# Optimization experiments

Hardware: AMD Instinct MI355X
Metric: run time of the kernel (lower is better)

## Reference

```python
import jax, jax.numpy as jnp
import numpy as np

E = 2048            # total edges in the batch
L = 8               # num_features == max_walk_length
G = 128             # num_graphs in the batch
HID = 128
N_NODES = 4096


def setup_inputs() -> dict:
    key = jax.random.key(0)
    k0, k1, k2, k3 = jax.random.split(key, 4)
    edge_index = jax.random.randint(k0, (2, E), 0, N_NODES, dtype=jnp.int32)
    edge_graph = jnp.sort(jax.random.randint(k1, (E,), 0, G, dtype=jnp.int32))
    W1 = jax.random.normal(k2, (L, HID), dtype=jnp.float32) * (1.0 / np.sqrt(L))
    b1 = jnp.zeros((HID,), dtype=jnp.float32)
    W2 = jax.random.normal(k3, (HID, 1), dtype=jnp.float32) * (1.0 / np.sqrt(HID))
    b2 = jnp.zeros((1,), dtype=jnp.float32)
    return {"edge_index": edge_index, "edge_graph": edge_graph,
            "W1": W1, "b1": b1, "W2": W2, "b2": b2}


def reference(edge_index, edge_graph, W1, b1, W2, b2):
    src, dst = edge_index[0], edge_index[1]  # edge i = (src_i, dst_i)
    # Non-backtracking edge matrix: B[i, j] = 1 iff dst_j == src_i and src_j != dst_i
    # (matches the python condition `u != l and v == k` with edge_i=(k,l), edge_j=(u,v))
    B = ((dst[None, :] == src[:, None]) & (src[None, :] != dst[:, None])).astype(jnp.float32)
    e = B.shape[0]
    walk_len = W1.shape[0]

    # B^1 .. B^L via scan, collecting diagonals (non-backtracking closed-walk counts per edge)
    def step(P, _):
        P = P @ B
        return P, jnp.diagonal(P)

    _, diags = jax.lax.scan(step, jnp.eye(e, dtype=jnp.float32), None, length=walk_len)
    # diags: [L, E] -> per-graph signatures [G, L]
    sig = jax.ops.segment_sum(diags.T, edge_graph, num_segments=G)

    # MLP (eval mode: dropout is identity)
    h = jax.nn.relu(sig @ W1 + b1)
    return h @ W2 + b2
```

## Files before the change

### kernel.cpp

```cpp
#include <hip/hip_runtime.h>


constexpr int E_EDGES  = 2048;
constexpr int L_WALK   = 8;
constexpr int G_GRAPHS = 128;
constexpr int HID      = 128;
constexpr int N_NODES  = 4096;
constexpr int BLOCK    = 1024;
constexpr int CAP      = 2048;

typedef unsigned long long u64;

__launch_bounds__(BLOCK, 1)
__global__ void nbc_all(const int* __restrict__ edge_index,
                        const int* __restrict__ edge_graph,
                        const float* __restrict__ W1,
                        const float* __restrict__ b1,
                        const float* __restrict__ W2,
                        const float* __restrict__ b2,
                        float* __restrict__ out)
{
    __shared__ u64 s_bufA[CAP];
    __shared__ u64 s_bufB[CAP];
    __shared__ u64 s_node[E_EDGES];
    __shared__ int s_sig[G_GRAPHS * L_WALK];
    __shared__ int s_nn[L_WALK + 1];
    __shared__ float s_W1[L_WALK * HID];
    __shared__ float s_b1[HID];
    __shared__ float s_W2[HID];
    __shared__ float s_b2;

    int* s_head = (int*)s_bufA;

    const int t    = threadIdx.x;
    const int lane = t & 63;

    const int2 se2 = ((const int2*)edge_index)[t];
    const int2 de2 = ((const int2*)(edge_index + E_EDGES))[t];
    const int2 ge2 = ((const int2*)edge_graph)[t];
    s_W1[t] = W1[t];
    if (t < HID) { s_b1[t] = b1[t]; s_W2[t] = W2[t]; }
    if (t == 0) s_b2 = b2[0];
    s_sig[t] = 0;
    if (t <= L_WALK) s_nn[t] = (t == 0) ? E_EDGES : 0;
    for (int n = t; n < N_NODES; n += BLOCK) s_head[n] = -1;
    __syncthreads();

    const int e0 = 2 * t, e1 = 2 * t + 1;
    {
        int prev0 = atomicExch(&s_head[de2.x], e0);
        s_node[e0] = (u64)se2.x | ((u64)de2.x << 12) | ((u64)(prev0 & 0xFFF) << 36);
        int prev1 = atomicExch(&s_head[de2.y], e1);
        s_node[e1] = (u64)se2.y | ((u64)de2.y << 12) | ((u64)(prev1 & 0xFFF) << 36);
    }
    __syncthreads();

    const int h0 = s_head[se2.x] & 0xFFF;
    const int h1 = s_head[se2.y] & 0xFFF;
    s_node[e0] |= (u64)h0 << 24;
    s_node[e1] |= (u64)h1 << 24;
    __syncthreads();
    s_bufA[e0] = (u64)e0 | ((u64)de2.x << 11) | ((u64)h0 << 23) | ((u64)ge2.x << 35);
    s_bufA[e1] = (u64)e1 | ((u64)de2.y << 11) | ((u64)h1 << 23) | ((u64)ge2.y << 35);
    __syncthreads();

    u64* cur = s_bufA;
    u64* nxt = s_bufB;
    for (int d = 0; d < L_WALK; ++d) {
        int n_cur = s_nn[d];
        if (n_cur > CAP) n_cur = CAP;
        for (int idx = t; idx < n_cur; idx += BLOCK) {
            u64 e = cur[idx];
            int s   = (int)( e        & 0x7FF);
            int dcc = (int)((e >> 11) & 0xFFF);
            int ptr = (int)((e >> 23) & 0xFFF);
            u64 gb  = e & (0x7Full << 35);
            while (ptr != 0xFFF) {
                u64 q = s_node[ptr];
                int sb = (int)(q & 0xFFF);
                int nx = (int)((q >> 36) & 0xFFF);
                if (sb != dcc) {
                    if (ptr == s)
                        atomicAdd(&s_sig[(int)(gb >> 35) * L_WALK + d], 1);
                    if (d < L_WALK - 1) {
                        u64 e2 = (u64)s | (((q >> 12) & 0xFFFFFFull) << 11) | gb;
                        u64 m = __ballot(1);
                        int leader = __ffsll(m) - 1;
                        int rank   = __popcll(m & ((1ull << lane) - 1ull));
                        int bpos = 0;
                        if (lane == leader) bpos = atomicAdd(&s_nn[d + 1], (int)__popcll(m));
                        bpos = __shfl(bpos, leader);
                        if (bpos + rank < CAP) nxt[bpos + rank] = e2;
                    }
                }
                ptr = nx;
            }
        }
        u64* tmp = cur; cur = nxt; nxt = tmp;
        __syncthreads();
    }

    float* s_part = (float*)s_node;
    {
        const int g   = t >> 3;
        const int sub = t & 7;
        float sv[L_WALK];
        #pragma unroll
        for (int k = 0; k < L_WALK; ++k) sv[k] = (float)s_sig[g * L_WALK + k];
        float o = 0.0f;
        const int j0 = sub * 16;
        #pragma unroll 4
        for (int jj = 0; jj < 16; ++jj) {
            int j = j0 + jj;
            float a = s_b1[j];
            #pragma unroll
            for (int k = 0; k < L_WALK; ++k) a += sv[k] * s_W1[k * HID + j];
            o += fmaxf(a, 0.0f) * s_W2[j];
        }
        s_part[t] = o;
    }
    __syncthreads();
    if (t < G_GRAPHS) {
        float r = s_b2;
        #pragma unroll
        for (int s = 0; s < 8; ++s) r += s_part[t * 8 + s];
        out[t] = r;
    }
}

extern "C" void kernel_launch(void* const* d_in, const int* in_sizes, int n_in,
                              void* d_out, int out_size, void* d_ws, size_t ws_size,
                              hipStream_t stream) {
    const int*   edge_index = (const int*)d_in[0];
    const int*   edge_graph = (const int*)d_in[1];
    const float* W1 = (const float*)d_in[2];
    const float* b1 = (const float*)d_in[3];
    const float* W2 = (const float*)d_in[4];
    const float* b2 = (const float*)d_in[5];
    float* out = (float*)d_out;

    nbc_all<<<1, BLOCK, 0, stream>>>(edge_index, edge_graph, W1, b1, W2, b2, out);
}
```

Before: 73.75 us.

## Halve block size, fuse first walk level into setup, finish small frontiers in one wave

Shrinks the single block from 1024 to 512 threads, with each thread now owning four edges. The first frontier expansion (depth 0) is done directly from registers with interleaved pointer chasing over four chains, so the initial buffer is never materialized. Once the frontier holds 64 or fewer entries, the remaining depths run on a single wavefront with no block-wide barriers, cutting the __syncthreads cost for the tail levels. The risk is less parallelism on large frontiers and some serialization in the single-wave tail.

After: 76.48 us. 3.7% more time.

```diff
diff --git a/kernel.cpp b/kernel.cpp
--- a/kernel.cpp
+++ b/kernel.cpp
@@ -1,17 +1,28 @@
 #include <hip/hip_runtime.h>
 
+
+typedef unsigned long long u64;
 
 constexpr int E_EDGES  = 2048;
 constexpr int L_WALK   = 8;
 constexpr int G_GRAPHS = 128;
 constexpr int HID      = 128;
 constexpr int N_NODES  = 4096;
-constexpr int BLOCK    = 1024;
+constexpr int TPB      = 512;
 constexpr int CAP      = 2048;
-
-typedef unsigned long long u64;
-
-__launch_bounds__(BLOCK, 1)
+constexpr int NIL      = 0xFFF;
+
+__device__ __forceinline__ void ballot_push(u64 e2, int lane, int* ctr, u64* buf) {
+    u64 m = __ballot(1);
+    int leader = __ffsll(m) - 1;
+    int rank   = __popcll(m & ((1ull << lane) - 1ull));
+    int bpos = 0;
+    if (lane == leader) bpos = atomicAdd(ctr, (int)__popcll(m));
+    bpos = __shfl(bpos, leader);
+    if (bpos + rank < CAP) buf[bpos + rank] = e2;
+}
+
+__launch_bounds__(TPB, 1)
 __global__ void nbc_all(const int* __restrict__ edge_index,
                         const int* __restrict__ edge_graph,
                         const float* __restrict__ W1,
@@ -34,63 +45,88 @@
 
     const int t    = threadIdx.x;
     const int lane = t & 63;
-
-    const int2 se2 = ((const int2*)edge_index)[t];
-    const int2 de2 = ((const int2*)(edge_index + E_EDGES))[t];
-    const int2 ge2 = ((const int2*)edge_graph)[t];
-    s_W1[t] = W1[t];
+    const int wave = t >> 6;
+
+    const int4 se4 = ((const int4*)edge_index)[t];
+    const int4 de4 = ((const int4*)(edge_index + E_EDGES))[t];
+    const int4 ge4 = ((const int4*)edge_graph)[t];
+    s_W1[t] = W1[t]; s_W1[t + TPB] = W1[t + TPB];
     if (t < HID) { s_b1[t] = b1[t]; s_W2[t] = W2[t]; }
     if (t == 0) s_b2 = b2[0];
-    s_sig[t] = 0;
-    if (t <= L_WALK) s_nn[t] = (t == 0) ? E_EDGES : 0;
-    for (int n = t; n < N_NODES; n += BLOCK) s_head[n] = -1;
-    __syncthreads();
-
-    const int e0 = 2 * t, e1 = 2 * t + 1;
+    s_sig[t] = 0; s_sig[t + TPB] = 0;
+    if (t <= L_WALK) s_nn[t] = 0;
+    #pragma unroll
+    for (int i = 0; i < 8; ++i) s_head[t + TPB * i] = -1;
+    __syncthreads();
+
+    int sev[4], dev[4], gev[4], prevv[4], hsv[4];
+    *(int4*)sev = se4; *(int4*)dev = de4; *(int4*)gev = ge4;
+
+    #pragma unroll
+    for (int i = 0; i < 4; ++i)
+        prevv[i] = atomicExch(&s_head[dev[i]], 4 * t + i);
+    __syncthreads();
+
+    #pragma unroll
+    for (int i = 0; i < 4; ++i) hsv[i] = s_head[sev[i]] & NIL;
+    #pragma unroll
+    for (int i = 0; i < 4; ++i)
+        s_node[4 * t + i] = (u64)sev[i] | ((u64)dev[i] << 12)
+                          | ((u64)hsv[i] << 24)
+                          | ((u64)(prevv[i] & NIL) << 36);
+    __syncthreads();
+
     {
-        int prev0 = atomicExch(&s_head[de2.x], e0);
-        s_node[e0] = (u64)se2.x | ((u64)de2.x << 12) | ((u64)(prev0 & 0xFFF) << 36);
-        int prev1 = atomicExch(&s_head[de2.y], e1);
-        s_node[e1] = (u64)se2.y | ((u64)de2.y << 12) | ((u64)(prev1 & 0xFFF) << 36);
-    }
-    __syncthreads();
-
-    const int h0 = s_head[se2.x] & 0xFFF;
-    const int h1 = s_head[se2.y] & 0xFFF;
-    s_node[e0] |= (u64)h0 << 24;
-    s_node[e1] |= (u64)h1 << 24;
-    __syncthreads();
-    s_bufA[e0] = (u64)e0 | ((u64)de2.x << 11) | ((u64)h0 << 23) | ((u64)ge2.x << 35);
-    s_bufA[e1] = (u64)e1 | ((u64)de2.y << 11) | ((u64)h1 << 23) | ((u64)ge2.y << 35);
+        int ptr4[4];
+        #pragma unroll
+        for (int i = 0; i < 4; ++i) ptr4[i] = hsv[i];
+        while ((ptr4[0] != NIL) | (ptr4[1] != NIL) | (ptr4[2] != NIL) | (ptr4[3] != NIL)) {
+            u64 q[4];
+            #pragma unroll
+            for (int i = 0; i < 4; ++i)
+                q[i] = (ptr4[i] != NIL) ? s_node[ptr4[i]] : 0;
+            #pragma unroll
+            for (int i = 0; i < 4; ++i) {
+                if (ptr4[i] != NIL) {
+                    int sb = (int)(q[i] & NIL);
+                    if (sb != dev[i]) {
+                        if (ptr4[i] == 4 * t + i)
+                            atomicAdd(&s_sig[gev[i] * L_WALK + 0], 1);
+                        u64 e2 = (u64)(4 * t + i)
+                               | (((q[i] >> 12) & 0xFFFFFFull) << 11)
+                               | ((u64)gev[i] << 35);
+                        ballot_push(e2, lane, &s_nn[1], s_bufA);
+                    }
+                    ptr4[i] = (int)((q[i] >> 36) & NIL);
+                }
+            }
+        }
+    }
     __syncthreads();
 
     u64* cur = s_bufA;
     u64* nxt = s_bufB;
-    for (int d = 0; d < L_WALK; ++d) {
+    int d = 1;
+    for (; d < L_WALK; ++d) {
         int n_cur = s_nn[d];
+        if (n_cur <= 64) break;
         if (n_cur > CAP) n_cur = CAP;
-        for (int idx = t; idx < n_cur; idx += BLOCK) {
+        for (int idx = t; idx < n_cur; idx += TPB) {
             u64 e = cur[idx];
             int s   = (int)( e        & 0x7FF);
-            int dcc = (int)((e >> 11) & 0xFFF);
-            int ptr = (int)((e >> 23) & 0xFFF);
+            int dcc = (int)((e >> 11) & NIL);
+            int ptr = (int)((e >> 23) & NIL);
             u64 gb  = e & (0x7Full << 35);
-            while (ptr != 0xFFF) {
+            while (ptr != NIL) {
                 u64 q = s_node[ptr];
-                int sb = (int)(q & 0xFFF);
-                int nx = (int)((q >> 36) & 0xFFF);
+                int sb = (int)(q & NIL);
+                int nx = (int)((q >> 36) & NIL);
                 if (sb != dcc) {
                     if (ptr == s)
                         atomicAdd(&s_sig[(int)(gb >> 35) * L_WALK + d], 1);
                     if (d < L_WALK - 1) {
                         u64 e2 = (u64)s | (((q >> 12) & 0xFFFFFFull) << 11) | gb;
-                        u64 m = __ballot(1);
-                        int leader = __ffsll(m) - 1;
-                        int rank   = __popcll(m & ((1ull << lane) - 1ull));
-                        int bpos = 0;
-                        if (lane == leader) bpos = atomicAdd(&s_nn[d + 1], (int)__popcll(m));
-                        bpos = __shfl(bpos, leader);
-                        if (bpos + rank < CAP) nxt[bpos + rank] = e2;
+                        ballot_push(e2, lane, &s_nn[d + 1], nxt);
                     }
                 }
                 ptr = nx;
@@ -100,10 +136,48 @@
         __syncthreads();
     }
 
+    if (d < L_WALK && wave == 0) {
+        volatile u64* vcur = cur;
+        volatile u64* vnxt = nxt;
+        for (; d < L_WALK; ++d) {
+            int n_cur = s_nn[d];
+            if (n_cur > CAP) n_cur = CAP;
+            for (int idx = lane; idx < n_cur; idx += 64) {
+                u64 e = vcur[idx];
+                int s   = (int)( e        & 0x7FF);
+                int dcc = (int)((e >> 11) & NIL);
+                int ptr = (int)((e >> 23) & NIL);
+                u64 gb  = e & (0x7Full << 35);
+                while (ptr != NIL) {
+                    u64 q = s_node[ptr];
+                    int sb = (int)(q & NIL);
+                    int nx = (int)((q >> 36) & NIL);
+                    if (sb != dcc) {
+                        if (ptr == s)
+                            atomicAdd(&s_sig[(int)(gb >> 35) * L_WALK + d], 1);
+                        if (d < L_WALK - 1) {
+                            u64 e2 = (u64)s | (((q >> 12) & 0xFFFFFFull) << 11) | gb;
+                            u64 m = __ballot(1);
+                            int leader = __ffsll(m) - 1;
+                            int rank   = __popcll(m & ((1ull << lane) - 1ull));
+                            int bpos = 0;
+                            if (lane == leader) bpos = atomicAdd(&s_nn[d + 1], (int)__popcll(m));
+                            bpos = __shfl(bpos, leader);
+                            if (bpos + rank < CAP) vnxt[bpos + rank] = e2;
+                        }
+                    }
+                    ptr = nx;
+                }
+            }
+            volatile u64* tmp = vcur; vcur = vnxt; vnxt = tmp;
+        }
+    }
+    __syncthreads();
+
     float* s_part = (float*)s_node;
-    {
-        const int g   = t >> 3;
-        const int sub = t & 7;
+    for (int slot = t; slot < G_GRAPHS * 8; slot += TPB) {
+        const int g   = slot >> 3;
+        const int sub = slot & 7;
         float sv[L_WALK];
         #pragma unroll
         for (int k = 0; k < L_WALK; ++k) sv[k] = (float)s_sig[g * L_WALK + k];
@@ -117,7 +191,7 @@
             for (int k = 0; k < L_WALK; ++k) a += sv[k] * s_W1[k * HID + j];
             o += fmaxf(a, 0.0f) * s_W2[j];
         }
-        s_part[t] = o;
+        s_part[slot] = o;
     }
     __syncthreads();
     if (t < G_GRAPHS) {
@@ -139,5 +213,5 @@
     const float* b2 = (const float*)d_in[5];
     float* out = (float*)d_out;
 
-    nbc_all<<<1, BLOCK, 0, stream>>>(edge_index, edge_graph, W1, b1, W2, b2, out);
+    nbc_all<<<1, TPB, 0, stream>>>(edge_index, edge_graph, W1, b1, W2, b2, out);
 }
```
